# Optimization experiments

Measured on AMD Instinct MI355X. Metric: run time of the kernel, lower is better.

## Reference

```python
import jax, jax.numpy as jnp
import numpy as np

E = 2048  # embed_size
H = 3     # heads (each full-width)


def setup_inputs() -> dict:
    key = jax.random.key(0)
    ks = jax.random.split(key, 6)
    B, N = 4, 2048
    x = jax.random.normal(ks[0], (B, N, E), dtype=jnp.float32)
    # torch Linear weights are [out, in]; y = x @ W.T. Stack the 3 heads.
    Wq = jax.random.normal(ks[1], (H, E, E), dtype=jnp.float32) * 0.02
    Wk = jax.random.normal(ks[2], (H, E, E), dtype=jnp.float32) * 0.02
    Wv = jax.random.normal(ks[3], (H, E, E), dtype=jnp.float32) * 0.02
    fc_w = jax.random.normal(ks[4], (E, E), dtype=jnp.float32) * 0.02
    fc_b = jax.random.normal(ks[5], (E,), dtype=jnp.float32) * 0.02
    return {"x": x, "Wq": Wq, "Wk": Wk, "Wv": Wv, "fc_w": fc_w, "fc_b": fc_b}


def reference(x, Wq, Wk, Wv, fc_w, fc_b):
    # Per-head full-width projections: [H, B, N, E]
    Q = jnp.einsum('bne,hde->hbnd', x, Wq)
    K = jnp.einsum('bne,hde->hbnd', x, Wk)
    V = jnp.einsum('bne,hde->hbnd', x, Wv)
    scale = 1.0 / jnp.sqrt(jnp.float32(E))
    # scores: [H, B, Nq, Nk]
    scores = jnp.einsum('hbnd,hbmd->hbnm', Q, K) * scale
    # Original uses torch.softmax(..., dim=1) on [B, Nq, Nk] -> query axis.
    # With leading head axis that is axis=2 here. Faithful reproduction.
    w = jax.nn.softmax(scores, axis=2)
    attn = jnp.einsum('hbnm,hbmd->hbnd', w, V)  # [H, B, N, E]
    mean = jnp.mean(attn, axis=0)               # [B, N, E]
    return mean @ fc_w.T + fc_b
```

## Files before the change

### kernel.cpp

```cpp
#include <hip/hip_runtime.h>
#include <stdint.h>

typedef __attribute__((ext_vector_type(4))) float floatx4;
typedef __bf16 bf16x8 __attribute__((ext_vector_type(8)));
typedef unsigned short ushort_t;

__device__ __forceinline__ ushort_t f2bf(float f) {
  unsigned u = __float_as_uint(f);
  u += 0x7FFFu + ((u >> 16) & 1u);
  return (ushort_t)(u >> 16);
}

__device__ __forceinline__ void gl_lds16(const void* g, void* l) {
  __builtin_amdgcn_global_load_lds(
      (__attribute__((address_space(1))) void*)g,
      (__attribute__((address_space(3))) void*)l, 16, 0, 0);
}

#define BAR() asm volatile("s_barrier" ::: "memory")
#define VM0() asm volatile("s_waitcnt vmcnt(0)" ::: "memory")
#define VM6() asm volatile("s_waitcnt vmcnt(6)" ::: "memory")

__global__ void cvt_f32_bf16(const float* __restrict__ src,
                             ushort_t* __restrict__ dst, long n) {
  long i = ((long)blockIdx.x * 256 + threadIdx.x) * 4;
  if (i >= n) return;
  float4 v = *(const float4*)(src + i);
  ushort4 o;
  o.x = f2bf(v.x); o.y = f2bf(v.y); o.z = f2bf(v.z); o.w = f2bf(v.w);
  *(ushort4*)(dst + i) = o;
}

template <int MODE>
__global__ __launch_bounds__(512, 2) void gemm256(
    const ushort_t* __restrict__ Abase, const ushort_t* __restrict__ Bbase,
    void* __restrict__ Cbase, const float* __restrict__ bias,
    int K, int lda, int ldb, int ldc,
    long strideA, long strideB, long strideC, float alpha) {
  __shared__ alignas(16) ushort_t sAB[2][2][256 * 64];

  const int z = blockIdx.z;
  const ushort_t* A = Abase + (long)z * strideA;
  const ushort_t* B = Bbase + (long)z * strideB;

  int bx, by;
  {
    const int gx = gridDim.x;
    const int nwg = gx * gridDim.y;
    const int f = blockIdx.x + gx * blockIdx.y;
    const int q = nwg >> 3, r = nwg & 7;
    const int xcd = f & 7, idx = f >> 3;
    const int fs = (xcd < r ? xcd * (q + 1) : r * (q + 1) + (xcd - r) * q) + idx;
    bx = fs % gx;
    by = fs / gx;
  }
  const int row0 = by * 256;
  const int col0 = bx * 256;

  const int tid  = threadIdx.x;
  const int lane = tid & 63;
  const int wave = tid >> 6;
  const int wm   = wave >> 2;
  const int wn   = wave & 3;

  const int fr = lane & 15;
  const int kq = lane >> 4;

  const int srow = lane >> 3;
  const int scol = ((lane & 7) ^ srow) * 8;

  const int kx0 = ((kq << 3)) ^ ((fr & 7) << 3);
  const int kx1 = ((1 << 5) | (kq << 3)) ^ ((fr & 7) << 3);

  const ushort_t* Ag = A + (long)(row0 + srow) * lda + scol;
  const ushort_t* Bg = B + (long)(col0 + srow) * ldb + scol;

  const floatx4 zero4 = {0.f, 0.f, 0.f, 0.f};
  floatx4 acc[8][4];
#pragma unroll
  for (int a = 0; a < 8; ++a)
#pragma unroll
    for (int b = 0; b < 4; ++b) acc[a][b] = zero4;

  const int nt = K >> 6;

  auto stA = [&](long kk, int buf, int qm) {
#pragma unroll
    for (int c = 0; c < 2; ++c) {
      const int rb = c * 128 + qm * 64 + wave * 8;
      gl_lds16(Ag + (long)rb * lda + kk, &sAB[buf][0][rb * 64]);
    }
  };
  auto stB = [&](long kk, int buf, int qn) {
#pragma unroll
    for (int c = 0; c < 2; ++c) {
      const int g = c * 8 + wave;
      const int rb = (g >> 2) * 64 + qn * 32 + (g & 3) * 8;
      gl_lds16(Bg + (long)rb * ldb + kk, &sAB[buf][1][rb * 64]);
    }
  };

  stA(0, 0, 0); stA(0, 0, 1); stB(0, 0, 0); stB(0, 0, 1);
  stA(64, 1, 0); stA(64, 1, 1); stB(64, 1, 0); stB(64, 1, 1);
  VM0();
  BAR();

#define MFMA_Q(QM, QN)                                                       \
  _Pragma("unroll") for (int mi = 0; mi < 4; ++mi)                           \
  _Pragma("unroll") for (int nj = 0; nj < 2; ++nj)                           \
  _Pragma("unroll") for (int ks = 0; ks < 2; ++ks)                           \
      acc[(QM)*4 + mi][(QN)*2 + nj] = __builtin_amdgcn_mfma_f32_16x16x32_bf16( \
          af[mi][ks], bq[nj][ks], acc[(QM)*4 + mi][(QN)*2 + nj], 0, 0, 0);

  const long kl = (long)(nt - 1) << 6;
  int cur = 0;
  for (int t = 0; t < nt; ++t) {
    const int nxt = cur ^ 1;
    long k1 = (long)(t + 1) << 6; if (k1 > kl) k1 = kl;
    long k2 = (long)(t + 2) << 6; if (k2 > kl) k2 = kl;
    const ushort_t* sA = sAB[cur][0];
    const ushort_t* sB = sAB[cur][1];
    bf16x8 af[4][2], bq[2][2];

#pragma unroll
    for (int mi = 0; mi < 4; ++mi) {
      const int rowb = (wm * 128 + mi * 16 + fr) * 64;
      af[mi][0] = *(const bf16x8*)&sA[rowb + kx0];
      af[mi][1] = *(const bf16x8*)&sA[rowb + kx1];
    }
#pragma unroll
    for (int nj = 0; nj < 2; ++nj) {
      const int rowb = (wn * 64 + nj * 16 + fr) * 64;
      bq[nj][0] = *(const bf16x8*)&sB[rowb + kx0];
      bq[nj][1] = *(const bf16x8*)&sB[rowb + kx1];
    }
    stB(k1, nxt, 0);
    BAR();
    __builtin_amdgcn_s_setprio(1);
    MFMA_Q(0, 0);
    __builtin_amdgcn_s_setprio(0);
    BAR();

#pragma unroll
    for (int nj = 0; nj < 2; ++nj) {
      const int rowb = (wn * 64 + 32 + nj * 16 + fr) * 64;
      bq[nj][0] = *(const bf16x8*)&sB[rowb + kx0];
      bq[nj][1] = *(const bf16x8*)&sB[rowb + kx1];
    }
    stA(k2, cur, 0);
    BAR();
    __builtin_amdgcn_s_setprio(1);
    MFMA_Q(0, 1);
    __builtin_amdgcn_s_setprio(0);
    BAR();

#pragma unroll
    for (int mi = 0; mi < 4; ++mi) {
      const int rowb = (wm * 128 + 64 + mi * 16 + fr) * 64;
      af[mi][0] = *(const bf16x8*)&sA[rowb + kx0];
      af[mi][1] = *(const bf16x8*)&sA[rowb + kx1];
    }
    BAR();
    __builtin_amdgcn_s_setprio(1);
    MFMA_Q(1, 1);
    __builtin_amdgcn_s_setprio(0);
    BAR();

#pragma unroll
    for (int nj = 0; nj < 2; ++nj) {
      const int rowb = (wn * 64 + nj * 16 + fr) * 64;
      bq[nj][0] = *(const bf16x8*)&sB[rowb + kx0];
      bq[nj][1] = *(const bf16x8*)&sB[rowb + kx1];
    }
    stB(k2, cur, 1);
    stA(k2, cur, 1);
    BAR();
    __builtin_amdgcn_s_setprio(1);
    MFMA_Q(1, 0);
    __builtin_amdgcn_s_setprio(0);
    VM6();
    BAR();

    cur = nxt;
  }
#undef MFMA_Q

  const int ccol  = lane & 15;
  const int crow4 = (lane >> 4) * 4;

  if (MODE == 0 || MODE == 3 || MODE == 4) {
    float* C = (float*)Cbase + (long)z * strideC;
#pragma unroll
    for (int a = 0; a < 8; ++a) {
      const int rbase = row0 + wm * 128 + (a >> 2) * 64 + (a & 3) * 16 + crow4;
#pragma unroll
      for (int b = 0; b < 4; ++b) {
        const int c = col0 + wn * 64 + (b >> 1) * 32 + (b & 1) * 16 + ccol;
        const float bb = (MODE == 3) ? bias[c] : 0.f;
#pragma unroll
        for (int r = 0; r < 4; ++r) {
          const long idx = (long)(rbase + r) * ldc + c;
          float v;
          if (MODE == 3)      v = acc[a][b][r] + bb;
          else if (MODE == 4) v = C[idx] + alpha * acc[a][b][r];
          else                v = alpha * acc[a][b][r];
          C[idx] = v;
        }
      }
    }
  } else {
    ushort_t* C = (ushort_t*)Cbase;
    const long QS = strideC;
#pragma unroll
    for (int a = 0; a < 8; ++a) {
      const int rbase = row0 + wm * 128 + (a >> 2) * 64 + (a & 3) * 16 + crow4;
#pragma unroll
      for (int b = 0; b < 4; ++b) {
        const int c = col0 + wn * 64 + (b >> 1) * 32 + (b & 1) * 16 + ccol;
#pragma unroll
        for (int r = 0; r < 4; ++r) {
          const int rr = rbase + r;
          const ushort_t v = f2bf(acc[a][b][r]);
          if (c < 2048)
            C[(long)rr * 2048 + c] = v;
          else if (c < 4096)
            C[QS + (long)rr * 2048 + (c - 2048)] = v;
          else
            C[2 * QS + (long)(rr >> 11) * 4194304 + (long)(c - 4096) * 2048 +
              (rr & 2047)] = v;
        }
      }
    }
  }
}

__global__ void softmax_cols(const float* __restrict__ Sbase,
                             ushort_t* __restrict__ wbase) {
  __shared__ float rmx[8][32], rsum[8][32];
  const long zoff = (long)blockIdx.y * 4194304;
  const int tx = threadIdx.x & 31;
  const int ty = threadIdx.x >> 5;
  const int m = blockIdx.x * 32 + tx;
  const float* Sm = Sbase + zoff + m;
  const int n0 = ty * 256;

  float mx = -3.0e38f, sum = 0.f;
#pragma unroll 4
  for (int n = n0; n < n0 + 256; ++n) {
    const float v = Sm[(long)n * 2048];
    if (v > mx) {
      sum = sum * __expf(mx - v) + 1.f;
      mx = v;
    } else {
      sum += __expf(v - mx);
    }
  }
  rmx[ty][tx] = mx;
  rsum[ty][tx] = sum;
  __syncthreads();
  float gm = rmx[0][tx];
#pragma unroll
  for (int s = 1; s < 8; ++s) gm = fmaxf(gm, rmx[s][tx]);
  float gs = 0.f;
#pragma unroll
  for (int s = 0; s < 8; ++s) gs += rsum[s][tx] * __expf(rmx[s][tx] - gm);
  const float inv = 1.f / gs;

  ushort_t* wm_ = wbase + zoff + m;
#pragma unroll 4
  for (int n = n0; n < n0 + 256; ++n)
    wm_[(long)n * 2048] = f2bf(__expf(Sm[(long)n * 2048] - gm) * inv);
}

extern "C" void kernel_launch(void* const* d_in, const int* in_sizes, int n_in,
                              void* d_out, int out_size, void* d_ws,
                              size_t ws_size, hipStream_t stream) {
  const float* x   = (const float*)d_in[0];
  const float* Wq  = (const float*)d_in[1];
  const float* Wk  = (const float*)d_in[2];
  const float* Wv  = (const float*)d_in[3];
  const float* fcw = (const float*)d_in[4];
  const float* fcb = (const float*)d_in[5];
  float* out = (float*)d_out;

  char* ws = (char*)d_ws;
  size_t off = 0;
  auto alloc = [&](size_t bytes) {
    char* p = ws + off;
    off += (bytes + 255) & ~(size_t)255;
    return p;
  };
  const long SL = 4194304L;
  const dim3 blk(256);
  const dim3 blk512(512);
  const float scale = 0.022097086912079608f;

  ushort_t* xb   = (ushort_t*)alloc(33554432);
  ushort_t* fcwb = (ushort_t*)alloc(8388608);
  float* mean32 = out;
  char* loop0 = ws + off;

  cvt_f32_bf16<<<16384, blk, 0, stream>>>(x, xb, 16777216L);
  cvt_f32_bf16<<<4096, blk, 0, stream>>>(fcw, fcwb, 4194304L);

  const bool big = ws_size >= 234881024ULL;

  if (big) {
    ushort_t* Wcat = (ushort_t*)alloc(25165824);
    ushort_t* Qh   = (ushort_t*)alloc(33554432);
    ushort_t* Kh   = (ushort_t*)alloc(33554432);
    ushort_t* Vth  = (ushort_t*)alloc(33554432);
    float*    S    = (float*)alloc(67108864);
    ushort_t* wc   = Qh;
    (void)Kh; (void)Vth;

    for (int h = 0; h < 3; ++h) {
      cvt_f32_bf16<<<4096, blk, 0, stream>>>(Wq + h * SL, Wcat, SL);
      cvt_f32_bf16<<<4096, blk, 0, stream>>>(Wk + h * SL, Wcat + SL, SL);
      cvt_f32_bf16<<<4096, blk, 0, stream>>>(Wv + h * SL, Wcat + 2 * SL, SL);

      gemm256<5><<<dim3(24, 32), blk512, 0, stream>>>(
          xb, Wcat, Qh, nullptr, 2048, 2048, 2048, 2048,
          0L, 0L, 16777216L, 1.0f);
      gemm256<0><<<dim3(8, 8, 4), blk512, 0, stream>>>(
          Qh, Qh + 16777216L, S, nullptr, 2048, 2048, 2048, 2048,
          SL, SL, SL, scale);
      softmax_cols<<<dim3(64, 4), blk, 0, stream>>>(S, wc);
      if (h == 0)
        gemm256<0><<<dim3(8, 8, 4), blk512, 0, stream>>>(
            wc, Qh + 33554432L, mean32, nullptr, 2048, 2048, 2048, 2048,
            SL, SL, SL, 1.0f / 3.0f);
      else
        gemm256<4><<<dim3(8, 8, 4), blk512, 0, stream>>>(
            wc, Qh + 33554432L, mean32, nullptr, 2048, 2048, 2048, 2048,
            SL, SL, SL, 1.0f / 3.0f);
    }
  } else {
    ushort_t* Wqh  = (ushort_t*)alloc(8388608);
    ushort_t* Wkh  = (ushort_t*)alloc(8388608);
    ushort_t* Wvh  = (ushort_t*)alloc(8388608);
    ushort_t* Qhb  = (ushort_t*)alloc(8388608);
    ushort_t* Khb  = (ushort_t*)alloc(8388608);
    ushort_t* Vthb = (ushort_t*)alloc(8388608);
    float*    S    = (float*)alloc(16777216);
    ushort_t* wchb = Qhb;
    (void)Wkh; (void)Wvh; (void)Khb; (void)Vthb;

    for (int h = 0; h < 3; ++h) {
      cvt_f32_bf16<<<4096, blk, 0, stream>>>(Wq + h * SL, Wqh, SL);
      cvt_f32_bf16<<<4096, blk, 0, stream>>>(Wk + h * SL, Wqh + SL, SL);
      cvt_f32_bf16<<<4096, blk, 0, stream>>>(Wv + h * SL, Wqh + 2 * SL, SL);

      for (int b = 0; b < 4; ++b) {
        const ushort_t* xbb = xb + b * SL;
        gemm256<5><<<dim3(24, 8), blk512, 0, stream>>>(
            xbb, Wqh, Qhb, nullptr, 2048, 2048, 2048, 2048,
            0L, 0L, 4194304L, 1.0f);
        gemm256<0><<<dim3(8, 8), blk512, 0, stream>>>(
            Qhb, Qhb + SL, S, nullptr, 2048, 2048, 2048, 2048,
            0L, 0L, 0L, scale);
        softmax_cols<<<dim3(64, 1), blk, 0, stream>>>(S, wchb);
        if (h == 0)
          gemm256<0><<<dim3(8, 8), blk512, 0, stream>>>(
              wchb, Qhb + 2 * SL, mean32 + b * SL, nullptr, 2048,
              2048, 2048, 2048, 0L, 0L, 0L, 1.0f / 3.0f);
        else
          gemm256<4><<<dim3(8, 8), blk512, 0, stream>>>(
              wchb, Qhb + 2 * SL, mean32 + b * SL, nullptr, 2048,
              2048, 2048, 2048, 0L, 0L, 0L, 1.0f / 3.0f);
      }
    }
  }

  ushort_t* meanb = (ushort_t*)loop0;
  cvt_f32_bf16<<<16384, blk, 0, stream>>>(mean32, meanb, 16777216L);
  gemm256<3><<<dim3(8, 32), blk512, 0, stream>>>(
      meanb, fcwb, out, fcb, 2048, 2048, 2048, 2048,
      0L, 0L, 0L, 1.0f);
}
```

Measured before the change: 1.847 ms.

## Unroll GEMM main loop by two with finer-grained A/B prefetch schedule

The 256x256 bf16 GEMM main loop is unrolled by two over the two LDS buffers with fixed buffer pointers. The B fragments of the first quadrant are kept in a second register set so they are reused in the last quadrant instead of being re-read from LDS. The global-to-LDS prefetches are spread evenly across the four MFMA phases, and the prologue waits on fewer outstanding loads. Explicit lgkmcnt waits are added before each MFMA block. This is meant to cut LDS reads and smooth memory issue, at the cost of more registers and an assumption that the K tile count is even.

```diff
diff --git a/kernel.cpp b/kernel.cpp
--- a/kernel.cpp
+++ b/kernel.cpp
@@ -20,6 +20,7 @@
 #define BAR() asm volatile("s_barrier" ::: "memory")
 #define VM0() asm volatile("s_waitcnt vmcnt(0)" ::: "memory")
 #define VM6() asm volatile("s_waitcnt vmcnt(6)" ::: "memory")
+#define LGK0() asm volatile("s_waitcnt lgkmcnt(0)" ::: "memory")
 
 __global__ void cvt_f32_bf16(const float* __restrict__ src,
                              ushort_t* __restrict__ dst, long n) {
@@ -84,105 +85,97 @@
 
   const int nt = K >> 6;
 
-  auto stA = [&](long kk, int buf, int qm) {
+  auto stA = [&](long kk, int buf, int h) {
 #pragma unroll
     for (int c = 0; c < 2; ++c) {
-      const int rb = c * 128 + qm * 64 + wave * 8;
+      const int rb = c * 128 + h * 64 + wave * 8;
       gl_lds16(Ag + (long)rb * lda + kk, &sAB[buf][0][rb * 64]);
     }
   };
-  auto stB = [&](long kk, int buf, int qn) {
+  auto stB = [&](long kk, int buf, int h) {
 #pragma unroll
     for (int c = 0; c < 2; ++c) {
       const int g = c * 8 + wave;
-      const int rb = (g >> 2) * 64 + qn * 32 + (g & 3) * 8;
+      const int rb = (g >> 2) * 64 + h * 32 + (g & 3) * 8;
       gl_lds16(Bg + (long)rb * ldb + kk, &sAB[buf][1][rb * 64]);
     }
   };
 
   stA(0, 0, 0); stA(0, 0, 1); stB(0, 0, 0); stB(0, 0, 1);
-  stA(64, 1, 0); stA(64, 1, 1); stB(64, 1, 0); stB(64, 1, 1);
-  VM0();
+  stA(64, 1, 0); stB(64, 1, 0); stB(64, 1, 1);
+  VM6();
   BAR();
 
-#define MFMA_Q(QM, QN)                                                       \
-  _Pragma("unroll") for (int mi = 0; mi < 4; ++mi)                           \
-  _Pragma("unroll") for (int nj = 0; nj < 2; ++nj)                           \
-  _Pragma("unroll") for (int ks = 0; ks < 2; ++ks)                           \
+#define RD_AF(SRC, QM)                                                        \
+  _Pragma("unroll") for (int mi = 0; mi < 4; ++mi) {                          \
+    const int rowb = (wm * 128 + (QM)*64 + mi * 16 + fr) * 64;                \
+    af[mi][0] = *(const bf16x8*)&(SRC)[rowb + kx0];                           \
+    af[mi][1] = *(const bf16x8*)&(SRC)[rowb + kx1];                           \
+  }
+#define RD_BQ(DST, SRC, QN)                                                   \
+  _Pragma("unroll") for (int nj = 0; nj < 2; ++nj) {                          \
+    const int rowb = (wn * 64 + (QN)*32 + nj * 16 + fr) * 64;                 \
+    DST[nj][0] = *(const bf16x8*)&(SRC)[rowb + kx0];                          \
+    DST[nj][1] = *(const bf16x8*)&(SRC)[rowb + kx1];                          \
+  }
+#define MFMA_Q(QM, QN, BQ)                                                    \
+  _Pragma("unroll") for (int mi = 0; mi < 4; ++mi)                            \
+  _Pragma("unroll") for (int nj = 0; nj < 2; ++nj)                            \
+  _Pragma("unroll") for (int ks = 0; ks < 2; ++ks)                            \
       acc[(QM)*4 + mi][(QN)*2 + nj] = __builtin_amdgcn_mfma_f32_16x16x32_bf16( \
-          af[mi][ks], bq[nj][ks], acc[(QM)*4 + mi][(QN)*2 + nj], 0, 0, 0);
+          af[mi][ks], BQ[nj][ks], acc[(QM)*4 + mi][(QN)*2 + nj], 0, 0, 0);
+#define PRIO1() __builtin_amdgcn_s_setprio(1)
+#define PRIO0() __builtin_amdgcn_s_setprio(0)
 
   const long kl = (long)(nt - 1) << 6;
-  int cur = 0;
-  for (int t = 0; t < nt; ++t) {
-    const int nxt = cur ^ 1;
-    long k1 = (long)(t + 1) << 6; if (k1 > kl) k1 = kl;
-    long k2 = (long)(t + 2) << 6; if (k2 > kl) k2 = kl;
-    const ushort_t* sA = sAB[cur][0];
-    const ushort_t* sB = sAB[cur][1];
-    bf16x8 af[4][2], bq[2][2];
-
-#pragma unroll
-    for (int mi = 0; mi < 4; ++mi) {
-      const int rowb = (wm * 128 + mi * 16 + fr) * 64;
-      af[mi][0] = *(const bf16x8*)&sA[rowb + kx0];
-      af[mi][1] = *(const bf16x8*)&sA[rowb + kx1];
-    }
-#pragma unroll
-    for (int nj = 0; nj < 2; ++nj) {
-      const int rowb = (wn * 64 + nj * 16 + fr) * 64;
-      bq[nj][0] = *(const bf16x8*)&sB[rowb + kx0];
-      bq[nj][1] = *(const bf16x8*)&sB[rowb + kx1];
-    }
-    stB(k1, nxt, 0);
-    BAR();
-    __builtin_amdgcn_s_setprio(1);
-    MFMA_Q(0, 0);
-    __builtin_amdgcn_s_setprio(0);
-    BAR();
-
-#pragma unroll
-    for (int nj = 0; nj < 2; ++nj) {
-      const int rowb = (wn * 64 + 32 + nj * 16 + fr) * 64;
-      bq[nj][0] = *(const bf16x8*)&sB[rowb + kx0];
-      bq[nj][1] = *(const bf16x8*)&sB[rowb + kx1];
-    }
-    stA(k2, cur, 0);
-    BAR();
-    __builtin_amdgcn_s_setprio(1);
-    MFMA_Q(0, 1);
-    __builtin_amdgcn_s_setprio(0);
-    BAR();
-
-#pragma unroll
-    for (int mi = 0; mi < 4; ++mi) {
-      const int rowb = (wm * 128 + 64 + mi * 16 + fr) * 64;
-      af[mi][0] = *(const bf16x8*)&sA[rowb + kx0];
-      af[mi][1] = *(const bf16x8*)&sA[rowb + kx1];
-    }
-    BAR();
-    __builtin_amdgcn_s_setprio(1);
-    MFMA_Q(1, 1);
-    __builtin_amdgcn_s_setprio(0);
-    BAR();
-
-#pragma unroll
-    for (int nj = 0; nj < 2; ++nj) {
-      const int rowb = (wn * 64 + nj * 16 + fr) * 64;
-      bq[nj][0] = *(const bf16x8*)&sB[rowb + kx0];
-      bq[nj][1] = *(const bf16x8*)&sB[rowb + kx1];
-    }
-    stB(k2, cur, 1);
-    stA(k2, cur, 1);
-    BAR();
-    __builtin_amdgcn_s_setprio(1);
-    MFMA_Q(1, 0);
-    __builtin_amdgcn_s_setprio(0);
+  const int niter = nt >> 1;
+  const ushort_t* sAu = sAB[0][0];
+  const ushort_t* sBu = sAB[0][1];
+  const ushort_t* sAv = sAB[1][0];
+  const ushort_t* sBv = sAB[1][1];
+
+  for (int i = 0; i < niter; ++i) {
+    const long kv = (long)(2 * i + 1) << 6;
+    long ku2 = (long)(2 * i + 2) << 6; if (ku2 > kl) ku2 = kl;
+    long kv2 = (long)(2 * i + 3) << 6; if (kv2 > kl) kv2 = kl;
+    bf16x8 af[4][2], bq0[2][2], bq1[2][2];
+
+    RD_AF(sAu, 0); RD_BQ(bq0, sBu, 0);
+    stA(kv, 1, 1);
+    BAR(); LGK0(); PRIO1(); MFMA_Q(0, 0, bq0); PRIO0(); BAR();
+
+    RD_BQ(bq1, sBu, 1);
+    stA(ku2, 0, 0);
+    BAR(); LGK0(); PRIO1(); MFMA_Q(0, 1, bq1); PRIO0(); BAR();
+
+    RD_AF(sAu, 1);
+    stB(ku2, 0, 0);
+    BAR(); LGK0(); PRIO1(); MFMA_Q(1, 1, bq1); PRIO0(); BAR();
+
+    stB(ku2, 0, 1);
+    BAR(); PRIO1(); MFMA_Q(1, 0, bq0); PRIO0();
     VM6();
     BAR();
 
-    cur = nxt;
-  }
+    RD_AF(sAv, 0); RD_BQ(bq0, sBv, 0);
+    stA(ku2, 0, 1);
+    BAR(); LGK0(); PRIO1(); MFMA_Q(0, 0, bq0); PRIO0(); BAR();
+
+    RD_BQ(bq1, sBv, 1);
+    stA(kv2, 1, 0);
+    BAR(); LGK0(); PRIO1(); MFMA_Q(0, 1, bq1); PRIO0(); BAR();
+
+    RD_AF(sAv, 1);
+    stB(kv2, 1, 0);
+    BAR(); LGK0(); PRIO1(); MFMA_Q(1, 1, bq1); PRIO0(); BAR();
+
+    stB(kv2, 1, 1);
+    BAR(); PRIO1(); MFMA_Q(1, 0, bq0); PRIO0();
+    VM6();
+    BAR();
+  }
+#undef RD_AF
+#undef RD_BQ
 #undef MFMA_Q
 
   const int ccol  = lane & 15;
```

Result: faster. 1.766 ms (-4.4%).
